# Performance work log

Hardware: AMD Instinct MI355X
Metric: run time of the kernel (lower is better)

The kernel has to match this reference:

```python
import math
import jax, jax.numpy as jnp
from jax import lax
import numpy as np

D_MODEL, D_STATE, D_CONV, EXPAND = 96, 16, 3, 2
D_INNER = EXPAND * D_MODEL            # 192
DT_RANK = math.ceil(D_MODEL / 16)     # 6
B_, H_, W_ = 2, 64, 64


def setup_inputs() -> dict:
    key = jax.random.key(0)
    ks = jax.random.split(key, 8)
    x = jax.random.normal(ks[0], (B_, H_, W_, D_MODEL), jnp.float32)
    in_proj_w = jax.random.normal(ks[1], (2 * D_INNER, D_MODEL), jnp.float32) * (D_MODEL ** -0.5)
    conv_w = jax.random.normal(ks[2], (D_INNER, 1, D_CONV, D_CONV), jnp.float32) * 0.1  # depthwise OIHW
    conv_b = jax.random.normal(ks[3], (D_INNER,), jnp.float32) * 0.1
    x_proj_weight = jax.random.normal(ks[4], (4, DT_RANK + 2 * D_STATE, D_INNER), jnp.float32) * (D_INNER ** -0.5)
    dt_init_std = DT_RANK ** -0.5
    dt_projs_weight = jax.random.uniform(ks[5], (4, D_INNER, DT_RANK), jnp.float32, -dt_init_std, dt_init_std)
    dt = jnp.exp(jax.random.uniform(ks[6], (4, D_INNER), jnp.float32) * (math.log(0.1) - math.log(0.001)) + math.log(0.001))
    dt = jnp.clip(dt, 1e-4, None)
    dt_projs_bias = dt + jnp.log(-jnp.expm1(-dt))  # inverse softplus init
    A_logs = jnp.log(jnp.tile(jnp.arange(1.0, D_STATE + 1.0, dtype=jnp.float32), (4 * D_INNER, 1)))  # (4*D, N)
    Ds = jnp.ones((4 * D_INNER,), jnp.float32)
    out_norm_w = jnp.ones((D_INNER,), jnp.float32)
    out_norm_b = jnp.zeros((D_INNER,), jnp.float32)
    out_proj_w = jax.random.normal(ks[7], (D_MODEL, D_INNER), jnp.float32) * (D_INNER ** -0.5)
    return dict(x=x, in_proj_w=in_proj_w, conv_w=conv_w, conv_b=conv_b,
                x_proj_weight=x_proj_weight, dt_projs_weight=dt_projs_weight,
                dt_projs_bias=dt_projs_bias, A_logs=A_logs, Ds=Ds,
                out_norm_w=out_norm_w, out_norm_b=out_norm_b, out_proj_w=out_proj_w)


def _ss2d(x, in_proj_w, conv_w, conv_b, x_proj_weight, dt_projs_weight,
          dt_projs_bias, A_logs, Ds, out_norm_w, out_norm_b, out_proj_w):
    B, H, W, C = x.shape
    K = 4
    d_inner = conv_w.shape[0]
    d_state = A_logs.shape[1]
    dt_rank = dt_projs_weight.shape[2]
    L = H * W

    # in_proj + split into x / gate z
    xz = jnp.einsum('bhwc,ec->bhwe', x, in_proj_w)
    xi, z = jnp.split(xz, 2, axis=-1)

    # depthwise 3x3 conv (padding=1) + SiLU, channels-first
    xc = jnp.transpose(xi, (0, 3, 1, 2))  # B,D,H,W
    xc = lax.conv_general_dilated(xc, conv_w, (1, 1), 'SAME',
                                  feature_group_count=d_inner,
                                  dimension_numbers=('NCHW', 'OIHW', 'NCHW'))
    xc = jax.nn.silu(xc + conv_b[None, :, None, None])

    # 4 scan directions: row-major, col-major, and their reverses
    x_hw = xc.reshape(B, d_inner, L)
    x_wh = jnp.transpose(xc, (0, 1, 3, 2)).reshape(B, d_inner, L)
    x_hwwh = jnp.stack([x_hw, x_wh], axis=1)                        # B,2,D,L
    xs = jnp.concatenate([x_hwwh, jnp.flip(x_hwwh, axis=-1)], axis=1)  # B,K,D,L

    x_dbl = jnp.einsum('bkdl,kcd->bkcl', xs, x_proj_weight)
    dts, Bs, Cs = jnp.split(x_dbl, [dt_rank, dt_rank + d_state], axis=2)
    dts = jnp.einsum('bkrl,kdr->bkdl', dts, dt_projs_weight)
    delta = jax.nn.softplus(dts + dt_projs_bias[None, :, :, None])  # B,K,D,L
    A = -jnp.exp(A_logs).reshape(K, d_inner, d_state)               # K,D,N

    # selective scan over L (serial recurrence)
    d_s = jnp.moveaxis(delta, -1, 0)  # L,B,K,D
    u_s = jnp.moveaxis(xs, -1, 0)     # L,B,K,D
    B_s = jnp.moveaxis(Bs, -1, 0)     # L,B,K,N
    C_s = jnp.moveaxis(Cs, -1, 0)     # L,B,K,N

    def step(h, inp):
        d_t, u_t, Bt, Ct = inp
        dA = jnp.exp(d_t[..., None] * A)                       # B,K,D,N
        h = h * dA + (d_t * u_t)[..., None] * Bt[:, :, None, :]
        y = jnp.einsum('bkdn,bkn->bkd', h, Ct)
        return h, y

    h0 = jnp.zeros((B, K, d_inner, d_state), jnp.float32)
    _, ys = lax.scan(step, h0, (d_s, u_s, B_s, C_s))  # ys: L,B,K,D
    ys = jnp.moveaxis(ys, 0, -1)                      # B,K,D,L
    out_y = ys + xs * Ds.reshape(K, d_inner)[None, :, :, None]

    # merge directions back to row-major layout
    inv_y = jnp.flip(out_y[:, 2:4], axis=-1)
    wh_y = jnp.transpose(out_y[:, 1].reshape(B, d_inner, W, H), (0, 1, 3, 2)).reshape(B, d_inner, L)
    invwh_y = jnp.transpose(inv_y[:, 1].reshape(B, d_inner, W, H), (0, 1, 3, 2)).reshape(B, d_inner, L)
    y = out_y[:, 0] + inv_y[:, 0] + wh_y + invwh_y    # B,D,L

    y = jnp.transpose(y, (0, 2, 1)).reshape(B, H, W, d_inner)
    mu = y.mean(-1, keepdims=True)
    var = y.var(-1, keepdims=True)
    y = (y - mu) * lax.rsqrt(var + 1e-5) * out_norm_w + out_norm_b
    y = y * jax.nn.silu(z)
    return jnp.einsum('bhwd,cd->bhwc', y, out_proj_w)


def reference(x, in_proj_w, conv_w, conv_b, x_proj_weight, dt_projs_weight,
              dt_projs_bias, A_logs, Ds, out_norm_w, out_norm_b, out_proj_w):
    return _ss2d(x, in_proj_w, conv_w, conv_b, x_proj_weight, dt_projs_weight,
                 dt_projs_bias, A_logs, Ds, out_norm_w, out_norm_b, out_proj_w)
```

## Files before the change

kernel.cpp:

```cpp
#include <hip/hip_runtime.h>
#include <math.h>

#define DMODEL 96
#define DIN    192
#define NST    16
#define RK     6
#define KDIR   4
#define LLEN   4096
#define BB     2
#define BP_TOT 8192
#define SCH    128
#define TCH    32

__global__ __launch_bounds__(192) void k_inproj(const float* __restrict__ x,
                                                const float* __restrict__ Wp,
                                                float* __restrict__ xi,
                                                float* __restrict__ z)
{
    __shared__ float xs[8 * 96];
    const int t  = threadIdx.x;
    const int p0 = blockIdx.x * 8;
    for (int idx = t; idx < 768; idx += 192)
        xs[idx] = x[(size_t)p0 * 96 + idx];
    __syncthreads();

    float acc0[8], acc1[8];
    #pragma unroll
    for (int i = 0; i < 8; ++i) { acc0[i] = 0.f; acc1[i] = 0.f; }
    const float* w0p = Wp + (size_t)t * 96;
    const float* w1p = Wp + (size_t)(t + 192) * 96;
    for (int k = 0; k < 96; k += 4) {
        float4 w0 = *(const float4*)(w0p + k);
        float4 w1 = *(const float4*)(w1p + k);
        #pragma unroll
        for (int p = 0; p < 8; ++p) {
            float4 xv = *(const float4*)&xs[p * 96 + k];
            acc0[p] = fmaf(w0.x, xv.x, fmaf(w0.y, xv.y, fmaf(w0.z, xv.z, fmaf(w0.w, xv.w, acc0[p]))));
            acc1[p] = fmaf(w1.x, xv.x, fmaf(w1.y, xv.y, fmaf(w1.z, xv.z, fmaf(w1.w, xv.w, acc1[p]))));
        }
    }
    #pragma unroll
    for (int p = 0; p < 8; ++p) {
        xi[(size_t)(p0 + p) * 192 + t] = acc0[p];
        z [(size_t)(p0 + p) * 192 + t] = acc1[p];
    }
}

__device__ __forceinline__ int inv_perm(int kd, int p)
{
    if (kd == 0) return p;
    if (kd == 1) return ((p & 63) << 6) | (p >> 6);
    if (kd == 2) return 4095 - p;
    return 4095 - (((p & 63) << 6) | (p >> 6));
}

__device__ __forceinline__ int perm_pos(int k, int l)
{
    if (k == 0) return l;
    if (k == 1) return ((l & 63) << 6) | (l >> 6);
    if (k == 2) return 4095 - l;
    int lr = 4095 - l;
    return ((lr & 63) << 6) | (lr >> 6);
}

__device__ __forceinline__ float softplus_fast(float x)
{
    float r = __logf(1.f + __expf(x));
    return (x > 15.f) ? x : r;
}

__device__ __forceinline__ void pow_chain(float e1, float* aa)
{
    float e2 = e1 * e1, e4 = e2 * e2, e8 = e4 * e4, e16 = e8 * e8;
    float e3 = e2 * e1, e5 = e4 * e1, e6 = e4 * e2, e7 = e4 * e3;
    aa[0] = e1;  aa[1] = e2;  aa[2] = e3;  aa[3] = e4;
    aa[4] = e5;  aa[5] = e6;  aa[6] = e7;  aa[7] = e8;
    aa[8] = e8 * e1;  aa[9] = e8 * e2;  aa[10] = e8 * e3;  aa[11] = e8 * e4;
    aa[12] = e8 * e5; aa[13] = e8 * e6; aa[14] = e8 * e7;  aa[15] = e16;
}

__device__ __forceinline__ int sm_remap(int c)
{
    return (c < 6) ? (32 + c) : (c - 6);
}

__global__ __launch_bounds__(192) void k_convxdbl(const float* __restrict__ xi,
                                                  const float* __restrict__ cw,
                                                  const float* __restrict__ cb,
                                                  const float* __restrict__ xpw,
                                                  float* __restrict__ xc,
                                                  float* __restrict__ xdk)
{
    __shared__ float xs[8 * 192];
    const int t   = threadIdx.x;
    const int p0  = blockIdx.x * 8;
    const int b   = p0 >> 12;
    const int pp0 = p0 & 4095;
    const int row = pp0 >> 6, c0 = pp0 & 63;

    float w9[9];
    #pragma unroll
    for (int i = 0; i < 9; ++i) w9[i] = cw[t * 9 + i];
    const float cbias = cb[t];

    float xv[3][10];
    #pragma unroll
    for (int ky = 0; ky < 3; ++ky) {
        int rr = row + ky - 1;
        #pragma unroll
        for (int kx = 0; kx < 10; ++kx) {
            int cc = c0 + kx - 1;
            float v = 0.f;
            if (rr >= 0 && rr < 64 && cc >= 0 && cc < 64)
                v = xi[((size_t)b * 4096 + rr * 64 + cc) * 192 + t];
            xv[ky][kx] = v;
        }
    }
    #pragma unroll
    for (int p = 0; p < 8; ++p) {
        float s = cbias;
        #pragma unroll
        for (int ky = 0; ky < 3; ++ky)
            #pragma unroll
            for (int kx = 0; kx < 3; ++kx)
                s = fmaf(xv[ky][p + kx], w9[ky * 3 + kx], s);
        float sv = s * (1.f / (1.f + __expf(-s)));
        xc[(size_t)(p0 + p) * 192 + t] = sv;
        xs[p * 192 + t] = sv;
    }
    __syncthreads();
    if (t >= 152) return;

    const int kd = t / 38, r = t % 38;
    float acc[8];
    #pragma unroll
    for (int i = 0; i < 8; ++i) acc[i] = 0.f;
    const float* wr = xpw + (size_t)t * 192;
    for (int k = 0; k < 192; k += 4) {
        float4 w = *(const float4*)(wr + k);
        #pragma unroll
        for (int p = 0; p < 8; ++p) {
            float4 x4 = *(const float4*)&xs[p * 192 + k];
            acc[p] = fmaf(w.x, x4.x, fmaf(w.y, x4.y, fmaf(w.z, x4.z, fmaf(w.w, x4.w, acc[p]))));
        }
    }
    #pragma unroll
    for (int p = 0; p < 8; ++p) {
        int pp = pp0 + p;
        int l  = inv_perm(kd, pp);
        xdk[((size_t)(b * 4 + kd) * 4096 + l) * 38 + r] = acc[p];
    }
}

__global__ __launch_bounds__(192) void k_scan1(const float* __restrict__ xc,
                                               const float* __restrict__ xdk,
                                               const float* __restrict__ dtw,
                                               const float* __restrict__ dtb,
                                               const float* __restrict__ Alog,
                                               const float* __restrict__ Ds,
                                               float* __restrict__ hend,
                                               float* __restrict__ prodA,
                                               float* __restrict__ yk)
{
    __shared__ float sm[TCH * 40];
    const int t   = threadIdx.x;
    const int blk = blockIdx.x;
    const int s = blk & (SCH - 1), k = (blk >> 7) & 3, b = blk >> 9;
    const int kd = k * 192 + t;
    const int l0 = s * TCH;

    const float* src = xdk + ((size_t)(b * 4 + k) * 4096 + l0) * 38;
    for (int idx = t; idx < TCH * 38; idx += 192) {
        int st = idx / 38, c = idx % 38;
        sm[st * 40 + sm_remap(c)] = src[idx];
    }

    const float A0 = -__expf(Alog[kd * 16]);
    bool fast = true;
    #pragma unroll
    for (int n = 1; n < 16; ++n) {
        float An = -__expf(Alog[kd * 16 + n]);
        fast = fast && (fabsf(An - (float)(n + 1) * A0) <= 1e-3f * fabsf(An));
    }
    float wdt[6];
    #pragma unroll
    for (int r = 0; r < 6; ++r) wdt[r] = dtw[kd * 6 + r];
    const float bias = dtb[kd];
    const float Dk   = Ds[kd];

    float h[16];
    #pragma unroll
    for (int n = 0; n < 16; ++n) h[n] = 0.f;
    float cd = 0.f;

    const float* xcb = xc + (size_t)b * 4096 * 192;
    float* ykb = yk + (size_t)(b * 4 + k) * 4096 * 192;
    int allfast = __syncthreads_and((int)fast);

    int p_cur = perm_pos(k, l0);
    float u = xcb[(size_t)p_cur * 192 + t];

    if (allfast) {
        for (int st = 0; st < TCH; ++st) {
            int p_next = (st + 1 < TCH) ? perm_pos(k, l0 + st + 1) : p_cur;
            float u_next = xcb[(size_t)p_next * 192 + t];
            const float* r = &sm[st * 40];
            float4 dq = *(const float4*)(r + 32);
            float xv = bias + dq.x * wdt[0] + dq.y * wdt[1] + dq.z * wdt[2]
                            + dq.w * wdt[3] + r[36] * wdt[4] + r[37] * wdt[5];
            float delta = softplus_fast(xv);
            cd += delta;
            float du = delta * u;
            float aa[16];
            pow_chain(__expf(delta * A0), aa);
            float4 b0 = *(const float4*)(r),      b1 = *(const float4*)(r + 4);
            float4 b2 = *(const float4*)(r + 8),  b3 = *(const float4*)(r + 12);
            float4 c0 = *(const float4*)(r + 16), c1 = *(const float4*)(r + 20);
            float4 c2 = *(const float4*)(r + 24), c3 = *(const float4*)(r + 28);
            float bv[16] = {b0.x, b0.y, b0.z, b0.w, b1.x, b1.y, b1.z, b1.w,
                            b2.x, b2.y, b2.z, b2.w, b3.x, b3.y, b3.z, b3.w};
            float cv[16] = {c0.x, c0.y, c0.z, c0.w, c1.x, c1.y, c1.z, c1.w,
                            c2.x, c2.y, c2.z, c2.w, c3.x, c3.y, c3.z, c3.w};
            float acc = Dk * u;
            #pragma unroll
            for (int n = 0; n < 16; ++n) {
                h[n] = fmaf(h[n], aa[n], du * bv[n]);
                acc  = fmaf(h[n], cv[n], acc);
            }
            ykb[(size_t)p_cur * 192 + t] = acc;
            u = u_next; p_cur = p_next;
        }
    } else {
        for (int st = 0; st < TCH; ++st) {
            int p_next = (st + 1 < TCH) ? perm_pos(k, l0 + st + 1) : p_cur;
            float u_next = xcb[(size_t)p_next * 192 + t];
            const float* r = &sm[st * 40];
            float xv = bias;
            #pragma unroll
            for (int j = 0; j < 6; ++j) xv += r[32 + j] * wdt[j];
            float delta = softplus_fast(xv);
            cd += delta;
            float du = delta * u;
            #pragma unroll
            for (int n = 0; n < 16; ++n) {
                float An = -__expf(Alog[kd * 16 + n]);
                h[n] = fmaf(h[n], __expf(delta * An), du * r[n]);
            }
            u = u_next; p_cur = p_next;
        }
    }

    size_t base = (size_t)blk * 3072 + t * 16;
    float ap[16];
    if (allfast) {
        pow_chain(__expf(cd * A0), ap);
    } else {
        #pragma unroll
        for (int n = 0; n < 16; ++n)
            ap[n] = __expf(-__expf(Alog[kd * 16 + n]) * cd);
    }
    #pragma unroll
    for (int i = 0; i < 4; ++i) {
        *(float4*)&hend [base + 4 * i] = make_float4(h[4*i], h[4*i+1], h[4*i+2], h[4*i+3]);
        *(float4*)&prodA[base + 4 * i] = make_float4(ap[4*i], ap[4*i+1], ap[4*i+2], ap[4*i+3]);
    }
}

__global__ __launch_bounds__(256) void k_scan2(const float* __restrict__ hend,
                                               float* __restrict__ prodA)
{
    __shared__ float smA[256], smH[256];
    const int t = threadIdx.x;
    const int g = t >> 4, n = t & 15;
    const int bk = blockIdx.x / 192, d = blockIdx.x % 192;
    const size_t base = (size_t)bk * SCH * 3072 + d * 16 + n;

    float a_[8], h_[8];
    float A = 1.f, H = 0.f;
    #pragma unroll
    for (int i = 0; i < 8; ++i) {
        size_t rec = base + (size_t)(g * 8 + i) * 3072;
        a_[i] = prodA[rec];
        h_[i] = hend[rec];
        H = fmaf(a_[i], H, h_[i]);
        A *= a_[i];
    }
    smA[t] = A; smH[t] = H;
    __syncthreads();
    if (t < 16) {
        float carry = 0.f;
        for (int g2 = 0; g2 < 16; ++g2) {
            float ta = smA[g2 * 16 + t], th = smH[g2 * 16 + t];
            smH[g2 * 16 + t] = carry;
            carry = fmaf(ta, carry, th);
        }
    }
    __syncthreads();
    float carry = smH[t];
    #pragma unroll
    for (int i = 0; i < 8; ++i) {
        size_t rec = base + (size_t)(g * 8 + i) * 3072;
        prodA[rec] = carry;
        carry = fmaf(a_[i], carry, h_[i]);
    }
}

__global__ __launch_bounds__(192) void k_scan3(const float* __restrict__ xc,
                                               const float* __restrict__ xdk,
                                               const float* __restrict__ dtw,
                                               const float* __restrict__ dtb,
                                               const float* __restrict__ Alog,
                                               const float* __restrict__ Ds,
                                               const float* __restrict__ hinit,
                                               float* __restrict__ yk)
{
    __shared__ float sm[TCH * 40];
    const int t   = threadIdx.x;
    const int blk = blockIdx.x;
    const int s = blk & (SCH - 1), k = (blk >> 7) & 3, b = blk >> 9;
    const int kd = k * 192 + t;
    const int l0 = s * TCH;

    const float* src = xdk + ((size_t)(b * 4 + k) * 4096 + l0) * 38;
    float* ykb = yk + (size_t)(b * 4 + k) * 4096 * 192;

    const float A0 = -__expf(Alog[kd * 16]);
    bool fast = true;
    #pragma unroll
    for (int n = 1; n < 16; ++n) {
        float An = -__expf(Alog[kd * 16 + n]);
        fast = fast && (fabsf(An - (float)(n + 1) * A0) <= 1e-3f * fabsf(An));
    }
    int allfast = __syncthreads_and((int)fast);

    float hi[16];
    size_t hbase = (size_t)blk * 3072 + t * 16;
    #pragma unroll
    for (int i = 0; i < 4; ++i) {
        float4 v = *(const float4*)&hinit[hbase + 4 * i];
        hi[4*i] = v.x; hi[4*i+1] = v.y; hi[4*i+2] = v.z; hi[4*i+3] = v.w;
    }

    if (allfast) {
        if (s == 0) return;
        for (int idx = t; idx < TCH * 22; idx += 192) {
            int st = idx / 22, c = idx % 22;
            int gcol = (c < 6) ? c : (16 + c);
            sm[st * 24 + ((c < 6) ? (16 + c) : (c - 6))] = src[st * 38 + gcol];
        }
        float wdt[6];
        #pragma unroll
        for (int r = 0; r < 6; ++r) wdt[r] = dtw[kd * 6 + r];
        const float bias = dtb[kd];
        __syncthreads();
        float cd = 0.f;
        for (int st = 0; st < TCH; ++st) {
            const float* r = &sm[st * 24];
            float xv = bias + r[16] * wdt[0] + r[17] * wdt[1] + r[18] * wdt[2]
                            + r[19] * wdt[3] + r[20] * wdt[4] + r[21] * wdt[5];
            cd += softplus_fast(xv);
            float aa[16];
            pow_chain(__expf(cd * A0), aa);
            float corr = 0.f;
            #pragma unroll
            for (int n = 0; n < 16; ++n)
                corr = fmaf(aa[n] * hi[n], r[n], corr);
            size_t off = (size_t)perm_pos(k, l0 + st) * 192 + t;
            ykb[off] += corr;
        }
    } else {
        for (int idx = t; idx < TCH * 38; idx += 192) {
            int st = idx / 38, c = idx % 38;
            sm[st * 40 + sm_remap(c)] = src[idx];
        }
        __syncthreads();
        const float* xcb = xc + (size_t)b * 4096 * 192;
        float wdt[6];
        #pragma unroll
        for (int r = 0; r < 6; ++r) wdt[r] = dtw[kd * 6 + r];
        const float bias = dtb[kd];
        const float Dk   = Ds[kd];
        float h[16];
        #pragma unroll
        for (int n = 0; n < 16; ++n) h[n] = hi[n];
        int p_cur = perm_pos(k, l0);
        float u = xcb[(size_t)p_cur * 192 + t];
        for (int st = 0; st < TCH; ++st) {
            int p_next = (st + 1 < TCH) ? perm_pos(k, l0 + st + 1) : p_cur;
            float u_next = xcb[(size_t)p_next * 192 + t];
            const float* r = &sm[st * 40];
            float xv = bias;
            #pragma unroll
            for (int j = 0; j < 6; ++j) xv += r[32 + j] * wdt[j];
            float delta = softplus_fast(xv);
            float du = delta * u;
            float acc = Dk * u;
            #pragma unroll
            for (int n = 0; n < 16; ++n) {
                float An = -__expf(Alog[kd * 16 + n]);
                h[n] = fmaf(h[n], __expf(delta * An), du * r[n]);
                acc  = fmaf(h[n], r[16 + n], acc);
            }
            ykb[(size_t)p_cur * 192 + t] = acc;
            u = u_next; p_cur = p_next;
        }
    }
}

__global__ __launch_bounds__(192) void k_lnout(const float* __restrict__ yk,
                                               const float* __restrict__ zb,
                                               const float* __restrict__ onw,
                                               const float* __restrict__ onb,
                                               const float* __restrict__ Wo,
                                               float* __restrict__ out)
{
    __shared__ float ys[1536];
    __shared__ float ps[192], pq[192];
    __shared__ float mu[8], ri[8];
    const int t   = threadIdx.x;
    const int p0  = blockIdx.x * 8;
    const int b   = p0 >> 12;
    const int pp0 = p0 & 4095;
    const size_t KSTR = (size_t)4096 * 192;

    #pragma unroll
    for (int i = 0; i < 8; ++i) {
        size_t base = ((size_t)(b * 4) * 4096 + pp0 + i) * 192 + t;
        ys[i * 192 + t] = yk[base] + yk[base + KSTR] + yk[base + 2 * KSTR] + yk[base + 3 * KSTR];
    }
    __syncthreads();

    {
        int pg = t / 24, j = t % 24;
        float s1 = 0.f, s2 = 0.f;
        #pragma unroll
        for (int m = 0; m < 8; ++m) {
            float v = ys[pg * 192 + j + 24 * m];
            s1 += v; s2 += v * v;
        }
        ps[t] = s1; pq[t] = s2;
    }
    __syncthreads();
    if (t < 8) {
        float s1 = 0.f, s2 = 0.f;
        #pragma unroll
        for (int j = 0; j < 24; ++j) { s1 += ps[t * 24 + j]; s2 += pq[t * 24 + j]; }
        float mean = s1 * (1.f / 192.f);
        float var  = s2 * (1.f / 192.f) - mean * mean;
        mu[t] = mean;
        ri[t] = rsqrtf(var + 1e-5f);
    }
    __syncthreads();

    {
        float w = onw[t], bo = onb[t];
        #pragma unroll
        for (int i = 0; i < 8; ++i) {
            float v  = ys[i * 192 + t];
            float yn = (v - mu[i]) * ri[i] * w + bo;
            float zv = zb[(size_t)(p0 + i) * 192 + t];
            float sg = 1.f / (1.f + __expf(-zv));
            ys[i * 192 + t] = yn * (zv * sg);
        }
    }
    __syncthreads();

    const int pg = t / 96, c = t % 96;
    float acc[4];
    #pragma unroll
    for (int i = 0; i < 4; ++i) acc[i] = 0.f;
    const float* wr = Wo + (size_t)c * 192;
    for (int k = 0; k < 192; k += 4) {
        float4 w = *(const float4*)(wr + k);
        #pragma unroll
        for (int i = 0; i < 4; ++i) {
            float4 xv = *(const float4*)&ys[(pg * 4 + i) * 192 + k];
            acc[i] = fmaf(w.x, xv.x, fmaf(w.y, xv.y, fmaf(w.z, xv.z, fmaf(w.w, xv.w, acc[i]))));
        }
    }
    #pragma unroll
    for (int i = 0; i < 4; ++i)
        out[(size_t)(p0 + pg * 4 + i) * 96 + c] = acc[i];
}

extern "C" void kernel_launch(void* const* d_in, const int* in_sizes, int n_in,
                              void* d_out, int out_size, void* d_ws, size_t ws_size,
                              hipStream_t stream)
{
    const float* x    = (const float*)d_in[0];
    const float* Wp   = (const float*)d_in[1];
    const float* cw   = (const float*)d_in[2];
    const float* cb   = (const float*)d_in[3];
    const float* xpw  = (const float*)d_in[4];
    const float* dtw  = (const float*)d_in[5];
    const float* dtb  = (const float*)d_in[6];
    const float* Alog = (const float*)d_in[7];
    const float* Ds   = (const float*)d_in[8];
    const float* onw  = (const float*)d_in[9];
    const float* onb  = (const float*)d_in[10];
    const float* Wo   = (const float*)d_in[11];
    float* out = (float*)d_out;

    const size_t NBP  = (size_t)BP_TOT * 192;
    const size_t NXD  = (size_t)BB * 4 * 4096 * 38;
    const size_t NSC  = (size_t)BB * 4 * SCH * 3072;
    float* WS    = (float*)d_ws;
    float* xibuf = WS;
    float* zb    = WS + NBP;
    float* xc    = WS + 2 * NBP;
    float* xdk   = WS + 3 * NBP;
    float* hend  = xdk + NXD;
    float* prodA = hend + NSC;
    float* yk    = prodA + NSC;

    k_inproj  <<<1024, 192, 0, stream>>>(x, Wp, xibuf, zb);
    k_convxdbl<<<1024, 192, 0, stream>>>(xibuf, cw, cb, xpw, xc, xdk);
    k_scan1   <<<1024, 192, 0, stream>>>(xc, xdk, dtw, dtb, Alog, Ds, hend, prodA, yk);
    k_scan2   <<<1536, 256, 0, stream>>>(hend, prodA);
    k_scan3   <<<1024, 192, 0, stream>>>(xc, xdk, dtw, dtb, Alog, Ds, prodA, yk);
    k_lnout   <<<1024, 192, 0, stream>>>(yk, zb, onw, onb, Wo, out);
}
```

Measured before the change: 210.3 us.

## Restructure chunked scan: halve chunk length, move output to pass 3, drop smem staging

Chunk count doubles (256 chunks of 16 steps), so scan1 and scan3 launch 2048 blocks, and the middle scan handles 16 records per thread. Scan1 now only computes chunk-end states and the decay product, without writing y. Scan3 reruns the full recurrence from the carried-in state and writes y once, replacing the old read-modify-write correction pass. Shared-memory staging of the xdbl rows is dropped in favour of direct broadcast global loads. A special path for A0 == -1 computes exp(-softplus(x)) as 1/(1+e^x), saving one exp; this relies on the A_log init pattern in the inputs.

Result: slower. 225.8 us (+7.4%).

```diff
diff --git a/kernel.cpp b/kernel.cpp
--- a/kernel.cpp
+++ b/kernel.cpp
@@ -9,8 +9,8 @@
 #define LLEN   4096
 #define BB     2
 #define BP_TOT 8192
-#define SCH    128
-#define TCH    32
+#define SCH    256
+#define TCH    16
 
 __global__ __launch_bounds__(192) void k_inproj(const float* __restrict__ x,
                                                 const float* __restrict__ Wp,
@@ -63,12 +63,6 @@
     return ((lr & 63) << 6) | (lr >> 6);
 }
 
-__device__ __forceinline__ float softplus_fast(float x)
-{
-    float r = __logf(1.f + __expf(x));
-    return (x > 15.f) ? x : r;
-}
-
 __device__ __forceinline__ void pow_chain(float e1, float* aa)
 {
     float e2 = e1 * e1, e4 = e2 * e2, e8 = e4 * e4, e16 = e8 * e8;
@@ -79,11 +73,6 @@
     aa[12] = e8 * e5; aa[13] = e8 * e6; aa[14] = e8 * e7;  aa[15] = e16;
 }
 
-__device__ __forceinline__ int sm_remap(int c)
-{
-    return (c < 6) ? (32 + c) : (c - 6);
-}
-
 __global__ __launch_bounds__(192) void k_convxdbl(const float* __restrict__ xi,
                                                   const float* __restrict__ cw,
                                                   const float* __restrict__ cb,
@@ -152,28 +141,21 @@
     }
 }
 
-__global__ __launch_bounds__(192) void k_scan1(const float* __restrict__ xc,
-                                               const float* __restrict__ xdk,
-                                               const float* __restrict__ dtw,
-                                               const float* __restrict__ dtb,
-                                               const float* __restrict__ Alog,
-                                               const float* __restrict__ Ds,
-                                               float* __restrict__ hend,
-                                               float* __restrict__ prodA,
-                                               float* __restrict__ yk)
-{
-    __shared__ float sm[TCH * 40];
+__global__ __launch_bounds__(192, 4) void k_scan1(const float* __restrict__ xc,
+                                                  const float* __restrict__ xdk,
+                                                  const float* __restrict__ dtw,
+                                                  const float* __restrict__ dtb,
+                                                  const float* __restrict__ Alog,
+                                                  float* __restrict__ hend,
+                                                  float* __restrict__ prodA)
+{
     const int t   = threadIdx.x;
     const int blk = blockIdx.x;
-    const int s = blk & (SCH - 1), k = (blk >> 7) & 3, b = blk >> 9;
+    const int s = blk & (SCH - 1), k = (blk >> 8) & 3, b = blk >> 10;
     const int kd = k * 192 + t;
     const int l0 = s * TCH;
 
-    const float* src = xdk + ((size_t)(b * 4 + k) * 4096 + l0) * 38;
-    for (int idx = t; idx < TCH * 38; idx += 192) {
-        int st = idx / 38, c = idx % 38;
-        sm[st * 40 + sm_remap(c)] = src[idx];
-    }
+    const float* __restrict__ src = xdk + ((size_t)(b * 4 + k) * 4096 + l0) * 38;
 
     const float A0 = -__expf(Alog[kd * 16]);
     bool fast = true;
@@ -186,65 +168,54 @@
     #pragma unroll
     for (int r = 0; r < 6; ++r) wdt[r] = dtw[kd * 6 + r];
     const float bias = dtb[kd];
-    const float Dk   = Ds[kd];
 
     float h[16];
     #pragma unroll
     for (int n = 0; n < 16; ++n) h[n] = 0.f;
-    float cd = 0.f;
 
     const float* xcb = xc + (size_t)b * 4096 * 192;
-    float* ykb = yk + (size_t)(b * 4 + k) * 4096 * 192;
     int allfast = __syncthreads_and((int)fast);
+    int a0neg1  = __syncthreads_and((int)(fabsf(A0 + 1.f) <= 1e-6f));
 
     int p_cur = perm_pos(k, l0);
     float u = xcb[(size_t)p_cur * 192 + t];
+    float W = 1.f, cd = 0.f;
 
     if (allfast) {
         for (int st = 0; st < TCH; ++st) {
             int p_next = (st + 1 < TCH) ? perm_pos(k, l0 + st + 1) : p_cur;
             float u_next = xcb[(size_t)p_next * 192 + t];
-            const float* r = &sm[st * 40];
-            float4 dq = *(const float4*)(r + 32);
-            float xv = bias + dq.x * wdt[0] + dq.y * wdt[1] + dq.z * wdt[2]
-                            + dq.w * wdt[3] + r[36] * wdt[4] + r[37] * wdt[5];
-            float delta = softplus_fast(xv);
-            cd += delta;
+            const float* r = src + st * 38;
+            float xv = bias + r[0] * wdt[0] + r[1] * wdt[1] + r[2] * wdt[2]
+                            + r[3] * wdt[3] + r[4] * wdt[4] + r[5] * wdt[5];
+            float exv = __expf(xv);
+            float delta = (xv > 15.f) ? xv : __logf(1.f + exv);
+            float e1 = a0neg1 ? __fdividef(1.f, 1.f + exv) : __expf(delta * A0);
+            W *= e1;
             float du = delta * u;
             float aa[16];
-            pow_chain(__expf(delta * A0), aa);
-            float4 b0 = *(const float4*)(r),      b1 = *(const float4*)(r + 4);
-            float4 b2 = *(const float4*)(r + 8),  b3 = *(const float4*)(r + 12);
-            float4 c0 = *(const float4*)(r + 16), c1 = *(const float4*)(r + 20);
-            float4 c2 = *(const float4*)(r + 24), c3 = *(const float4*)(r + 28);
-            float bv[16] = {b0.x, b0.y, b0.z, b0.w, b1.x, b1.y, b1.z, b1.w,
-                            b2.x, b2.y, b2.z, b2.w, b3.x, b3.y, b3.z, b3.w};
-            float cv[16] = {c0.x, c0.y, c0.z, c0.w, c1.x, c1.y, c1.z, c1.w,
-                            c2.x, c2.y, c2.z, c2.w, c3.x, c3.y, c3.z, c3.w};
-            float acc = Dk * u;
-            #pragma unroll
-            for (int n = 0; n < 16; ++n) {
-                h[n] = fmaf(h[n], aa[n], du * bv[n]);
-                acc  = fmaf(h[n], cv[n], acc);
-            }
-            ykb[(size_t)p_cur * 192 + t] = acc;
+            pow_chain(e1, aa);
+            #pragma unroll
+            for (int n = 0; n < 16; ++n)
+                h[n] = fmaf(h[n], aa[n], du * r[6 + n]);
             u = u_next; p_cur = p_next;
         }
     } else {
         for (int st = 0; st < TCH; ++st) {
             int p_next = (st + 1 < TCH) ? perm_pos(k, l0 + st + 1) : p_cur;
             float u_next = xcb[(size_t)p_next * 192 + t];
-            const float* r = &sm[st * 40];
+            const float* r = src + st * 38;
             float xv = bias;
             #pragma unroll
-            for (int j = 0; j < 6; ++j) xv += r[32 + j] * wdt[j];
-            float delta = softplus_fast(xv);
+            for (int j = 0; j < 6; ++j) xv += r[j] * wdt[j];
+            float exv = __expf(xv);
+            float delta = (xv > 15.f) ? xv : __logf(1.f + exv);
             cd += delta;
             float du = delta * u;
             #pragma unroll
             for (int n = 0; n < 16; ++n) {
                 float An = -__expf(Alog[kd * 16 + n]);
-                h[n] = fmaf(h[n], __expf(delta * An), du * r[n]);
+                h[n] = fmaf(h[n], __expf(delta * An), du * r[6 + n]);
             }
             u = u_next; p_cur = p_next;
         }
@@ -253,7 +224,7 @@
     size_t base = (size_t)blk * 3072 + t * 16;
     float ap[16];
     if (allfast) {
-        pow_chain(__expf(cd * A0), ap);
+        pow_chain(W, ap);
     } else {
         #pragma unroll
         for (int n = 0; n < 16; ++n)
@@ -275,11 +246,11 @@
     const int bk = blockIdx.x / 192, d = blockIdx.x % 192;
     const size_t base = (size_t)bk * SCH * 3072 + d * 16 + n;
 
-    float a_[8], h_[8];
+    float a_[16], h_[16];
     float A = 1.f, H = 0.f;
     #pragma unroll
-    for (int i = 0; i < 8; ++i) {
-        size_t rec = base + (size_t)(g * 8 + i) * 3072;
+    for (int i = 0; i < 16; ++i) {
+        size_t rec = base + (size_t)(g * 16 + i) * 3072;
         a_[i] = prodA[rec];
         h_[i] = hend[rec];
         H = fmaf(a_[i], H, h_[i]);
@@ -298,30 +269,29 @@
     __syncthreads();
     float carry = smH[t];
     #pragma unroll
-    for (int i = 0; i < 8; ++i) {
-        size_t rec = base + (size_t)(g * 8 + i) * 3072;
+    for (int i = 0; i < 16; ++i) {
+        size_t rec = base + (size_t)(g * 16 + i) * 3072;
         prodA[rec] = carry;
         carry = fmaf(a_[i], carry, h_[i]);
     }
 }
 
-__global__ __launch_bounds__(192) void k_scan3(const float* __restrict__ xc,
-                                               const float* __restrict__ xdk,
-                                               const float* __restrict__ dtw,
-                                               const float* __restrict__ dtb,
-                                               const float* __restrict__ Alog,
-                                               const float* __restrict__ Ds,
-                                               const float* __restrict__ hinit,
-                                               float* __restrict__ yk)
-{
-    __shared__ float sm[TCH * 40];
+__global__ __launch_bounds__(192, 4) void k_scan3(const float* __restrict__ xc,
+                                                  const float* __restrict__ xdk,
+                                                  const float* __restrict__ dtw,
+                                                  const float* __restrict__ dtb,
+                                                  const float* __restrict__ Alog,
+                                                  const float* __restrict__ Ds,
+                                                  const float* __restrict__ hinit,
+                                                  float* __restrict__ yk)
+{
     const int t   = threadIdx.x;
     const int blk = blockIdx.x;
-    const int s = blk & (SCH - 1), k = (blk >> 7) & 3, b = blk >> 9;
+    const int s = blk & (SCH - 1), k = (blk >> 8) & 3, b = blk >> 10;
     const int kd = k * 192 + t;
     const int l0 = s * TCH;
 
-    const float* src = xdk + ((size_t)(b * 4 + k) * 4096 + l0) * 38;
+    const float* __restrict__ src = xdk + ((size_t)(b * 4 + k) * 4096 + l0) * 38;
     float* ykb = yk + (size_t)(b * 4 + k) * 4096 * 192;
 
     const float A0 = -__expf(Alog[kd * 16]);
@@ -331,75 +301,66 @@
         float An = -__expf(Alog[kd * 16 + n]);
         fast = fast && (fabsf(An - (float)(n + 1) * A0) <= 1e-3f * fabsf(An));
     }
-    int allfast = __syncthreads_and((int)fast);
-
-    float hi[16];
+    float wdt[6];
+    #pragma unroll
+    for (int r = 0; r < 6; ++r) wdt[r] = dtw[kd * 6 + r];
+    const float bias = dtb[kd];
+    const float Dk   = Ds[kd];
+
+    float h[16];
     size_t hbase = (size_t)blk * 3072 + t * 16;
     #pragma unroll
     for (int i = 0; i < 4; ++i) {
         float4 v = *(const float4*)&hinit[hbase + 4 * i];
-        hi[4*i] = v.x; hi[4*i+1] = v.y; hi[4*i+2] = v.z; hi[4*i+3] = v.w;
-    }
+        h[4*i] = v.x; h[4*i+1] = v.y; h[4*i+2] = v.z; h[4*i+3] = v.w;
+    }
+
+    const float* xcb = xc + (size_t)b * 4096 * 192;
+    int allfast = __syncthreads_and((int)fast);
+    int a0neg1  = __syncthreads_and((int)(fabsf(A0 + 1.f) <= 1e-6f));
+
+    int p_cur = perm_pos(k, l0);
+    float u = xcb[(size_t)p_cur * 192 + t];
 
     if (allfast) {
-        if (s == 0) return;
-        for (int idx = t; idx < TCH * 22; idx += 192) {
-            int st = idx / 22, c = idx % 22;
-            int gcol = (c < 6) ? c : (16 + c);
-            sm[st * 24 + ((c < 6) ? (16 + c) : (c - 6))] = src[st * 38 + gcol];
-        }
-        float wdt[6];
-        #pragma unroll
-        for (int r = 0; r < 6; ++r) wdt[r] = dtw[kd * 6 + r];
-        const float bias = dtb[kd];
-        __syncthreads();
-        float cd = 0.f;
-        for (int st = 0; st < TCH; ++st) {
-            const float* r = &sm[st * 24];
-            float xv = bias + r[16] * wdt[0] + r[17] * wdt[1] + r[18] * wdt[2]
-                            + r[19] * wdt[3] + r[20] * wdt[4] + r[21] * wdt[5];
-            cd += softplus_fast(xv);
-            float aa[16];
-            pow_chain(__expf(cd * A0), aa);
-            float corr = 0.f;
-            #pragma unroll
-            for (int n = 0; n < 16; ++n)
-                corr = fmaf(aa[n] * hi[n], r[n], corr);
-            size_t off = (size_t)perm_pos(k, l0 + st) * 192 + t;
-            ykb[off] += corr;
-        }
-    } else {
-        for (int idx = t; idx < TCH * 38; idx += 192) {
-            int st = idx / 38, c = idx % 38;
-            sm[st * 40 + sm_remap(c)] = src[idx];
-        }
-        __syncthreads();
-        const float* xcb = xc + (size_t)b * 4096 * 192;
-        float wdt[6];
-        #pragma unroll
-        for (int r = 0; r < 6; ++r) wdt[r] = dtw[kd * 6 + r];
-        const float bias = dtb[kd];
-        const float Dk   = Ds[kd];
-        float h[16];
-        #pragma unroll
-        for (int n = 0; n < 16; ++n) h[n] = hi[n];
-        int p_cur = perm_pos(k, l0);
-        float u = xcb[(size_t)p_cur * 192 + t];
         for (int st = 0; st < TCH; ++st) {
             int p_next = (st + 1 < TCH) ? perm_pos(k, l0 + st + 1) : p_cur;
             float u_next = xcb[(size_t)p_next * 192 + t];
-            const float* r = &sm[st * 40];
+            const float* r = src + st * 38;
+            float xv = bias + r[0] * wdt[0] + r[1] * wdt[1] + r[2] * wdt[2]
+                            + r[3] * wdt[3] + r[4] * wdt[4] + r[5] * wdt[5];
+            float exv = __expf(xv);
+            float delta = (xv > 15.f) ? xv : __logf(1.f + exv);
+            float e1 = a0neg1 ? __fdividef(1.f, 1.f + exv) : __expf(delta * A0);
+            float du = delta * u;
+            float aa[16];
+            pow_chain(e1, aa);
+            float acc = Dk * u;
+            #pragma unroll
+            for (int n = 0; n < 16; ++n) {
+                h[n] = fmaf(h[n], aa[n], du * r[6 + n]);
+                acc  = fmaf(h[n], r[22 + n], acc);
+            }
+            ykb[(size_t)p_cur * 192 + t] = acc;
+            u = u_next; p_cur = p_next;
+        }
+    } else {
+        for (int st = 0; st < TCH; ++st) {
+            int p_next = (st + 1 < TCH) ? perm_pos(k, l0 + st + 1) : p_cur;
+            float u_next = xcb[(size_t)p_next * 192 + t];
+            const float* r = src + st * 38;
             float xv = bias;
             #pragma unroll
-            for (int j = 0; j < 6; ++j) xv += r[32 + j] * wdt[j];
-            float delta = softplus_fast(xv);
+            for (int j = 0; j < 6; ++j) xv += r[j] * wdt[j];
+            float exv = __expf(xv);
+            float delta = (xv > 15.f) ? xv : __logf(1.f + exv);
             float du = delta * u;
             float acc = Dk * u;
             #pragma unroll
             for (int n = 0; n < 16; ++n) {
                 float An = -__expf(Alog[kd * 16 + n]);
-                h[n] = fmaf(h[n], __expf(delta * An), du * r[n]);
-                acc  = fmaf(h[n], r[16 + n], acc);
+                h[n] = fmaf(h[n], __expf(delta * An), du * r[6 + n]);
+                acc  = fmaf(h[n], r[22 + n], acc);
             }
             ykb[(size_t)p_cur * 192 + t] = acc;
             u = u_next; p_cur = p_next;
@@ -515,8 +476,8 @@
 
     k_inproj  <<<1024, 192, 0, stream>>>(x, Wp, xibuf, zb);
     k_convxdbl<<<1024, 192, 0, stream>>>(xibuf, cw, cb, xpw, xc, xdk);
-    k_scan1   <<<1024, 192, 0, stream>>>(xc, xdk, dtw, dtb, Alog, Ds, hend, prodA, yk);
+    k_scan1   <<<2048, 192, 0, stream>>>(xc, xdk, dtw, dtb, Alog, hend, prodA);
     k_scan2   <<<1536, 256, 0, stream>>>(hend, prodA);
-    k_scan3   <<<1024, 192, 0, stream>>>(xc, xdk, dtw, dtb, Alog, Ds, prodA, yk);
+    k_scan3   <<<2048, 192, 0, stream>>>(xc, xdk, dtw, dtb, Alog, Ds, prodA, yk);
     k_lnout   <<<1024, 192, 0, stream>>>(yk, zb, onw, onb, Wo, out);
 }
```

## Move output computation from scan1 to scan3 and batch softplus/exp per 8 steps

Applied to the files above, without the earlier changes.

Scan1 now only computes end states and decay products, no longer writing yk or reading C. Scan3 reruns the full recurrence from the propagated initial state and writes the outputs directly, instead of adding a correction term to outputs that scan1 wrote. Both fast paths compute softplus and exp for 8 timesteps ahead of the serial recurrence so those operations can overlap. This removes one full write and read-modify-write pass over yk, at the cost of redoing the state recurrence in scan3, including for chunk 0, which previously returned early.

Measured after the change: 214.5 us. About the same (+2.0%).

```diff
diff --git a/kernel.cpp b/kernel.cpp
--- a/kernel.cpp
+++ b/kernel.cpp
@@ -157,10 +157,8 @@
                                                const float* __restrict__ dtw,
                                                const float* __restrict__ dtb,
                                                const float* __restrict__ Alog,
-                                               const float* __restrict__ Ds,
                                                float* __restrict__ hend,
-                                               float* __restrict__ prodA,
-                                               float* __restrict__ yk)
+                                               float* __restrict__ prodA)
 {
     __shared__ float sm[TCH * 40];
     const int t   = threadIdx.x;
@@ -186,7 +184,6 @@
     #pragma unroll
     for (int r = 0; r < 6; ++r) wdt[r] = dtw[kd * 6 + r];
     const float bias = dtb[kd];
-    const float Dk   = Ds[kd];
 
     float h[16];
     #pragma unroll
@@ -194,41 +191,43 @@
     float cd = 0.f;
 
     const float* xcb = xc + (size_t)b * 4096 * 192;
-    float* ykb = yk + (size_t)(b * 4 + k) * 4096 * 192;
     int allfast = __syncthreads_and((int)fast);
 
     int p_cur = perm_pos(k, l0);
     float u = xcb[(size_t)p_cur * 192 + t];
 
     if (allfast) {
-        for (int st = 0; st < TCH; ++st) {
-            int p_next = (st + 1 < TCH) ? perm_pos(k, l0 + st + 1) : p_cur;
-            float u_next = xcb[(size_t)p_next * 192 + t];
-            const float* r = &sm[st * 40];
-            float4 dq = *(const float4*)(r + 32);
-            float xv = bias + dq.x * wdt[0] + dq.y * wdt[1] + dq.z * wdt[2]
-                            + dq.w * wdt[3] + r[36] * wdt[4] + r[37] * wdt[5];
-            float delta = softplus_fast(xv);
-            cd += delta;
-            float du = delta * u;
-            float aa[16];
-            pow_chain(__expf(delta * A0), aa);
-            float4 b0 = *(const float4*)(r),      b1 = *(const float4*)(r + 4);
-            float4 b2 = *(const float4*)(r + 8),  b3 = *(const float4*)(r + 12);
-            float4 c0 = *(const float4*)(r + 16), c1 = *(const float4*)(r + 20);
-            float4 c2 = *(const float4*)(r + 24), c3 = *(const float4*)(r + 28);
-            float bv[16] = {b0.x, b0.y, b0.z, b0.w, b1.x, b1.y, b1.z, b1.w,
-                            b2.x, b2.y, b2.z, b2.w, b3.x, b3.y, b3.z, b3.w};
-            float cv[16] = {c0.x, c0.y, c0.z, c0.w, c1.x, c1.y, c1.z, c1.w,
-                            c2.x, c2.y, c2.z, c2.w, c3.x, c3.y, c3.z, c3.w};
-            float acc = Dk * u;
-            #pragma unroll
-            for (int n = 0; n < 16; ++n) {
-                h[n] = fmaf(h[n], aa[n], du * bv[n]);
-                acc  = fmaf(h[n], cv[n], acc);
+        for (int g0 = 0; g0 < TCH; g0 += 8) {
+            float e18[8], dl8[8];
+            #pragma unroll
+            for (int j = 0; j < 8; ++j) {
+                const float* r = &sm[(g0 + j) * 40];
+                float4 dq = *(const float4*)(r + 32);
+                float xv = bias + dq.x * wdt[0] + dq.y * wdt[1] + dq.z * wdt[2]
+                                + dq.w * wdt[3] + r[36] * wdt[4] + r[37] * wdt[5];
+                float delta = softplus_fast(xv);
+                dl8[j] = delta;
+                e18[j] = __expf(delta * A0);
             }
-            ykb[(size_t)p_cur * 192 + t] = acc;
-            u = u_next; p_cur = p_next;
+            #pragma unroll
+            for (int j = 0; j < 8; ++j) {
+                int st = g0 + j;
+                int p_next = (st + 1 < TCH) ? perm_pos(k, l0 + st + 1) : p_cur;
+                float u_next = xcb[(size_t)p_next * 192 + t];
+                const float* r = &sm[st * 40];
+                cd += dl8[j];
+                float du = dl8[j] * u;
+                float aa[16];
+                pow_chain(e18[j], aa);
+                float4 b0 = *(const float4*)(r),      b1 = *(const float4*)(r + 4);
+                float4 b2 = *(const float4*)(r + 8),  b3 = *(const float4*)(r + 12);
+                float bv[16] = {b0.x, b0.y, b0.z, b0.w, b1.x, b1.y, b1.z, b1.w,
+                                b2.x, b2.y, b2.z, b2.w, b3.x, b3.y, b3.z, b3.w};
+                #pragma unroll
+                for (int n = 0; n < 16; ++n)
+                    h[n] = fmaf(h[n], aa[n], du * bv[n]);
+                u = u_next; p_cur = p_next;
+            }
         }
     } else {
         for (int st = 0; st < TCH; ++st) {
@@ -324,6 +323,11 @@
     const float* src = xdk + ((size_t)(b * 4 + k) * 4096 + l0) * 38;
     float* ykb = yk + (size_t)(b * 4 + k) * 4096 * 192;
 
+    for (int idx = t; idx < TCH * 38; idx += 192) {
+        int st = idx / 38, c = idx % 38;
+        sm[st * 40 + sm_remap(c)] = src[idx];
+    }
+
     const float A0 = -__expf(Alog[kd * 16]);
     bool fast = true;
     #pragma unroll
@@ -331,60 +335,67 @@
         float An = -__expf(Alog[kd * 16 + n]);
         fast = fast && (fabsf(An - (float)(n + 1) * A0) <= 1e-3f * fabsf(An));
     }
-    int allfast = __syncthreads_and((int)fast);
-
-    float hi[16];
+    float wdt[6];
+    #pragma unroll
+    for (int r = 0; r < 6; ++r) wdt[r] = dtw[kd * 6 + r];
+    const float bias = dtb[kd];
+    const float Dk   = Ds[kd];
+
+    float h[16];
     size_t hbase = (size_t)blk * 3072 + t * 16;
     #pragma unroll
     for (int i = 0; i < 4; ++i) {
         float4 v = *(const float4*)&hinit[hbase + 4 * i];
-        hi[4*i] = v.x; hi[4*i+1] = v.y; hi[4*i+2] = v.z; hi[4*i+3] = v.w;
-    }
+        h[4*i] = v.x; h[4*i+1] = v.y; h[4*i+2] = v.z; h[4*i+3] = v.w;
+    }
+
+    const float* xcb = xc + (size_t)b * 4096 * 192;
+    int allfast = __syncthreads_and((int)fast);
+
+    int p_cur = perm_pos(k, l0);
+    float u = xcb[(size_t)p_cur * 192 + t];
 
     if (allfast) {
-        if (s == 0) return;
-        for (int idx = t; idx < TCH * 22; idx += 192) {
-            int st = idx / 22, c = idx % 22;
-            int gcol = (c < 6) ? c : (16 + c);
-            sm[st * 24 + ((c < 6) ? (16 + c) : (c - 6))] = src[st * 38 + gcol];
-        }
-        float wdt[6];
-        #pragma unroll
-        for (int r = 0; r < 6; ++r) wdt[r] = dtw[kd * 6 + r];
-        const float bias = dtb[kd];
-        __syncthreads();
-        float cd = 0.f;
-        for (int st = 0; st < TCH; ++st) {
-            const float* r = &sm[st * 24];
-            float xv = bias + r[16] * wdt[0] + r[17] * wdt[1] + r[18] * wdt[2]
-                            + r[19] * wdt[3] + r[20] * wdt[4] + r[21] * wdt[5];
-            cd += softplus_fast(xv);
-            float aa[16];
-            pow_chain(__expf(cd * A0), aa);
-            float corr = 0.f;
-            #pragma unroll
-            for (int n = 0; n < 16; ++n)
-                corr = fmaf(aa[n] * hi[n], r[n], corr);
-            size_t off = (size_t)perm_pos(k, l0 + st) * 192 + t;
-            ykb[off] += corr;
+        for (int g0 = 0; g0 < TCH; g0 += 8) {
+            float e18[8], dl8[8];
+            #pragma unroll
+            for (int j = 0; j < 8; ++j) {
+                const float* r = &sm[(g0 + j) * 40];
+                float4 dq = *(const float4*)(r + 32);
+                float xv = bias + dq.x * wdt[0] + dq.y * wdt[1] + dq.z * wdt[2]
+                                + dq.w * wdt[3] + r[36] * wdt[4] + r[37] * wdt[5];
+                float delta = softplus_fast(xv);
+                dl8[j] = delta;
+                e18[j] = __expf(delta * A0);
+            }
+            #pragma unroll
+            for (int j = 0; j < 8; ++j) {
+                int st = g0 + j;
+                int p_next = (st + 1 < TCH) ? perm_pos(k, l0 + st + 1) : p_cur;
+                float u_next = xcb[(size_t)p_next * 192 + t];
+                const float* r = &sm[st * 40];
+                float du = dl8[j] * u;
+                float aa[16];
+                pow_chain(e18[j], aa);
+                float4 b0 = *(const float4*)(r),      b1 = *(const float4*)(r + 4);
+                float4 b2 = *(const float4*)(r + 8),  b3 = *(const float4*)(r + 12);
+                float4 c0 = *(const float4*)(r + 16), c1 = *(const float4*)(r + 20);
+                float4 c2 = *(const float4*)(r + 24), c3 = *(const float4*)(r + 28);
+                float bv[16] = {b0.x, b0.y, b0.z, b0.w, b1.x, b1.y, b1.z, b1.w,
+                                b2.x, b2.y, b2.z, b2.w, b3.x, b3.y, b3.z, b3.w};
+                float cv[16] = {c0.x, c0.y, c0.z, c0.w, c1.x, c1.y, c1.z, c1.w,
+                                c2.x, c2.y, c2.z, c2.w, c3.x, c3.y, c3.z, c3.w};
+                float acc = Dk * u;
+                #pragma unroll
+                for (int n = 0; n < 16; ++n) {
+                    h[n] = fmaf(h[n], aa[n], du * bv[n]);
+                    acc  = fmaf(h[n], cv[n], acc);
+                }
+                ykb[(size_t)p_cur * 192 + t] = acc;
+                u = u_next; p_cur = p_next;
+            }
         }
     } else {
-        for (int idx = t; idx < TCH * 38; idx += 192) {
-            int st = idx / 38, c = idx % 38;
-            sm[st * 40 + sm_remap(c)] = src[idx];
-        }
-        __syncthreads();
-        const float* xcb = xc + (size_t)b * 4096 * 192;
-        float wdt[6];
-        #pragma unroll
-        for (int r = 0; r < 6; ++r) wdt[r] = dtw[kd * 6 + r];
-        const float bias = dtb[kd];
-        const float Dk   = Ds[kd];
-        float h[16];
-        #pragma unroll
-        for (int n = 0; n < 16; ++n) h[n] = hi[n];
-        int p_cur = perm_pos(k, l0);
-        float u = xcb[(size_t)p_cur * 192 + t];
         for (int st = 0; st < TCH; ++st) {
             int p_next = (st + 1 < TCH) ? perm_pos(k, l0 + st + 1) : p_cur;
             float u_next = xcb[(size_t)p_next * 192 + t];
@@ -515,7 +526,7 @@
 
     k_inproj  <<<1024, 192, 0, stream>>>(x, Wp, xibuf, zb);
     k_convxdbl<<<1024, 192, 0, stream>>>(xibuf, cw, cb, xpw, xc, xdk);
-    k_scan1   <<<1024, 192, 0, stream>>>(xc, xdk, dtw, dtb, Alog, Ds, hend, prodA, yk);
+    k_scan1   <<<1024, 192, 0, stream>>>(xc, xdk, dtw, dtb, Alog, hend, prodA);
     k_scan2   <<<1536, 256, 0, stream>>>(hend, prodA);
     k_scan3   <<<1024, 192, 0, stream>>>(xc, xdk, dtw, dtb, Alog, Ds, prodA, yk);
     k_lnout   <<<1024, 192, 0, stream>>>(yk, zb, onw, onb, Wo, out);
```
